# Kernel tuning notes

Measured on AMD Instinct MI355X. Metric: run time of the kernel, lower is better.

Reference implementation:

```python
import jax, jax.numpy as jnp
import numpy as np

B, TQ, TK = 2, 2048, 2048
D, H, G = 1024, 16, 4
HD = D // H  # 64
MAX_LEN = 4096


def _rope(x, max_len):
    # x: [B, H, S, hd]; interleaved even/odd RoPE, freqs use full head_dim in denom
    hd = x.shape[-1]
    seq = x.shape[2]
    pos = jnp.arange(max_len, dtype=jnp.float32)[:, None]           # [max_len, 1]
    div = jnp.exp(jnp.arange(0, hd, 2, dtype=jnp.float32) * (-np.log(10000.0) / hd))
    sin = jnp.sin(pos * div)[:seq]                                   # [S, hd/2]
    cos = jnp.cos(pos * div)[:seq]
    xe, xo = x[..., 0::2], x[..., 1::2]
    oe = xe * cos - xo * sin
    oo = xe * sin + xo * cos
    return jnp.stack([oe, oo], axis=-1).reshape(x.shape)


def setup_inputs() -> dict:
    key = jax.random.key(0)
    ks = jax.random.split(key, 10)
    s = 0.02
    return {
        "X": jax.random.normal(ks[0], (B, TQ, D), jnp.float32),
        "encoder_output": jax.random.normal(ks[1], (B, TK, D), jnp.float32),
        "Wq": jax.random.normal(ks[2], (D, D), jnp.float32) * s,
        "bq": jnp.zeros((D,), jnp.float32),
        "Wk": jax.random.normal(ks[3], (D, G * HD), jnp.float32) * s,
        "bk": jnp.zeros((G * HD,), jnp.float32),
        "Wv": jax.random.normal(ks[4], (D, G * HD), jnp.float32) * s,
        "bv": jnp.zeros((G * HD,), jnp.float32),
        "Wo": jax.random.normal(ks[5], (D, D), jnp.float32) * s,
        "bo": jnp.zeros((D,), jnp.float32),
        "max_len": MAX_LEN,
    }


def reference(X, encoder_output, Wq, bq, Wk, bk, Wv, bv, Wo, bo, max_len):
    bsz, tq, d = X.shape
    q = X @ Wq + bq                       # [B, TQ, D]
    k = encoder_output @ Wk + bk          # [B, TK, G*HD]
    v = encoder_output @ Wv + bv

    q = q.reshape(bsz, tq, H, HD).transpose(0, 2, 1, 3)          # [B, H, TQ, HD]
    k = k.reshape(bsz, -1, G, HD).transpose(0, 2, 1, 3)          # [B, G, TK, HD]
    v = v.reshape(bsz, -1, G, HD).transpose(0, 2, 1, 3)
    # expand each group to H//G consecutive heads (matches torch expand+reshape)
    k = jnp.repeat(k, H // G, axis=1)                            # [B, H, TK, HD]
    v = jnp.repeat(v, H // G, axis=1)

    q = _rope(q, max_len)
    k = _rope(k, max_len)

    scores = jnp.einsum("bhqd,bhkd->bhqk", q, k) / jnp.sqrt(jnp.float32(HD))
    w = jax.nn.softmax(scores, axis=-1)
    o = jnp.einsum("bhqk,bhkd->bhqd", w, v)                      # [B, H, TQ, HD]
    o = o.transpose(0, 2, 1, 3).reshape(bsz, tq, d)
    return o @ Wo + bo
```

## Files before the change

kernel.cpp:

```cpp
#include <hip/hip_runtime.h>
#include <cstdint>


typedef __bf16 bf16x8 __attribute__((ext_vector_type(8)));
typedef __bf16 bf16x4v __attribute__((ext_vector_type(4)));
typedef float f32x4 __attribute__((ext_vector_type(4)));

#define MFMA16(a, b, c) __builtin_amdgcn_mfma_f32_16x16x32_bf16((a), (b), (c), 0, 0, 0)

constexpr int Bc = 2, TQc = 2048, TKc = 2048, Dc = 1024, Hc = 16, Gc = 4, HDc = 64;
constexpr float QSCALE = 0.18033688011112042f;

__device__ __forceinline__ ushort bfbits(float x) {
  __bf16 h = (__bf16)x;
  return __builtin_bit_cast(ushort, h);
}

__device__ __forceinline__ float fexp2(float x) {
  float r;
  asm("v_exp_f32 %0, %1" : "=v"(r) : "v"(x));
  return r;
}

__device__ __forceinline__ float fmax3(float a, float b, float c) {
  return fmaxf(fmaxf(a, b), c);
}

__device__ __forceinline__ void async_lds16(void* lds, const void* g) {
  __builtin_amdgcn_global_load_lds((const __attribute__((address_space(1))) uint32_t*)g,
                                   (__attribute__((address_space(3))) uint32_t*)lds,
                                   16, 0, 0);
}

__global__ __launch_bounds__(256) void prep_k(const float* __restrict__ X,
                                              const float* __restrict__ E,
                                              const float* __restrict__ Wq,
                                              const float* __restrict__ Wo,
                                              const float* __restrict__ Wk,
                                              const float* __restrict__ Wv,
                                              ushort* __restrict__ Xb,
                                              ushort* __restrict__ Eb,
                                              ushort* __restrict__ Wqt,
                                              ushort* __restrict__ Wot,
                                              ushort* __restrict__ Wkvt) {
  __shared__ float t[64][65];
  const int bid = blockIdx.x;
  if (bid < 8192) {
    const float* s = (bid < 4096) ? X : E;
    ushort* d = (bid < 4096) ? Xb : Eb;
    int i = (bid & 4095) * 256 + threadIdx.x;
    float4 v = reinterpret_cast<const float4*>(s)[i];
    ushort4 o;
    o.x = bfbits(v.x); o.y = bfbits(v.y); o.z = bfbits(v.z); o.w = bfbits(v.w);
    reinterpret_cast<ushort4*>(d)[i] = o;
    return;
  }
  const int w = bid - 8192;
  const int z = w >> 8, rem = w & 255;
  const int bx = rem & 15, by = rem >> 4;
  const float* src;
  ushort* dst;
  int C, c0;
  if (z == 0)      { src = Wq; dst = Wqt; C = 1024; c0 = bx * 64; }
  else if (z == 1) { src = Wo; dst = Wot; C = 1024; c0 = bx * 64; }
  else {
    if (bx >= 8) return;
    if (bx < 4) { src = Wk; dst = Wkvt; }
    else        { src = Wv; dst = Wkvt + 256 * 1024; }
    C = 256; c0 = (bx & 3) * 64;
  }
  const int r0 = by * 64;
  const int tx = threadIdx.x & 63, ty = threadIdx.x >> 6;
#pragma unroll
  for (int i = 0; i < 16; ++i) {
    int r = i * 4 + ty;
    t[r][tx] = src[(size_t)(r0 + r) * C + c0 + tx];
  }
  __syncthreads();
#pragma unroll
  for (int i = 0; i < 16; ++i) {
    int c = i * 4 + ty;
    dst[(size_t)(c0 + c) * 1024 + r0 + tx] = bfbits(t[tx][c]);
  }
}

__device__ __forceinline__ void gemm_mainloop(const ushort* __restrict__ A,
                                              const ushort* __restrict__ Bt,
                                              int m0, int n0, int K,
                                              char* sA, char* sB,
                                              f32x4 acc[4][2]) {
  const int lane = threadIdx.x & 63, wid = threadIdx.x >> 6;
  const int l15 = lane & 15, l4 = lane >> 4;
  const int wr = (wid >> 1) * 64, wc = (wid & 1) * 32;
  const int srow = lane >> 3;
  const int scc = (lane & 7) ^ (srow & 7);
  const int rxr = l15 & 7;

  const int nsteps = K >> 6;
#pragma unroll
  for (int j = 0; j < 4; ++j) {
    int c = wid * 4 + j;
    async_lds16(sA + c * 1024, A + (size_t)(m0 + c * 8 + srow) * K + scc * 8);
  }
#pragma unroll
  for (int j = 0; j < 2; ++j) {
    int c = wid * 2 + j;
    async_lds16(sB + c * 1024, Bt + (size_t)(n0 + c * 8 + srow) * K + scc * 8);
  }
  __syncthreads();

  int buf = 0;
  for (int s2 = 0; s2 < nsteps; ++s2) {
    if (s2 + 1 < nsteps) {
      const int k0 = (s2 + 1) * 64;
      char* dA = sA + (buf ^ 1) * 16384;
      char* dB = sB + (buf ^ 1) * 8192;
#pragma unroll
      for (int j = 0; j < 4; ++j) {
        int c = wid * 4 + j;
        async_lds16(dA + c * 1024, A + (size_t)(m0 + c * 8 + srow) * K + k0 + scc * 8);
      }
#pragma unroll
      for (int j = 0; j < 2; ++j) {
        int c = wid * 2 + j;
        async_lds16(dB + c * 1024, Bt + (size_t)(n0 + c * 8 + srow) * K + k0 + scc * 8);
      }
    }
    const char* aB = sA + buf * 16384;
    const char* bB = sB + buf * 8192;
    bf16x8 af[2][4], bfr[2][2];
#pragma unroll
    for (int mi = 0; mi < 4; ++mi) {
      const int row = wr + mi * 16 + l15;
#pragma unroll
      for (int kk = 0; kk < 2; ++kk)
        af[kk][mi] = *reinterpret_cast<const bf16x8*>(
            aB + row * 128 + (((l4 + kk * 4) ^ rxr) << 4));
    }
#pragma unroll
    for (int ni = 0; ni < 2; ++ni) {
      const int row = wc + ni * 16 + l15;
#pragma unroll
      for (int kk = 0; kk < 2; ++kk)
        bfr[kk][ni] = *reinterpret_cast<const bf16x8*>(
            bB + row * 128 + (((l4 + kk * 4) ^ rxr) << 4));
    }
#pragma unroll
    for (int kk = 0; kk < 2; ++kk)
#pragma unroll
      for (int mi = 0; mi < 4; ++mi)
#pragma unroll
        for (int ni = 0; ni < 2; ++ni)
          acc[mi][ni] = MFMA16(af[kk][mi], bfr[kk][ni], acc[mi][ni]);
    __syncthreads();
    buf ^= 1;
  }
}

__device__ __forceinline__ void gemm_epilogue(f32x4 acc[4][2], int mode, int m0,
                                              int n0, const float* b0,
                                              const float* b1, float* Cf,
                                              ushort* U0, ushort* U1, int N) {
  const int lane = threadIdx.x & 63, wid = threadIdx.x >> 6;
  const int l15 = lane & 15, l4 = lane >> 4;
  const int wr = (wid >> 1) * 64, wc = (wid & 1) * 32;
#pragma unroll
  for (int ni = 0; ni < 2; ++ni) {
    const int col = n0 + wc + ni * 16 + l15;
    if (mode == 0) {
      const float bv = b0[col];
#pragma unroll
      for (int mi = 0; mi < 4; ++mi) {
        const int rowb = m0 + wr + mi * 16 + l4 * 4;
#pragma unroll
        for (int r = 0; r < 4; ++r)
          Cf[(size_t)(rowb + r) * N + col] = acc[mi][ni][r] + bv;
      }
    } else if (mode == 1) {
      const int h = col >> 6, d = col & 63, fi = d >> 1, odd = d & 1;
      const float div = __expf(-0.28782313662425572f * (float)fi);
      const float bv = b0[col];
#pragma unroll
      for (int mi = 0; mi < 4; ++mi) {
        const int rowb = m0 + wr + mi * 16 + l4 * 4;
#pragma unroll
        for (int r = 0; r < 4; ++r) {
          const int row = rowb + r, b = row >> 11, t = row & 2047;
          const float val = acc[mi][ni][r] + bv;
          const float prt = __shfl_xor(val, 1);
          float sn, cs;
          __sincosf((float)t * div, &sn, &cs);
          const float o = odd ? (prt * sn + val * cs) : (val * cs - prt * sn);
          U0[(((size_t)(b * Hc + h)) * TQc + t) * HDc + d] = bfbits(o * QSCALE);
        }
      }
    } else {
      if (col < 256) {
        const int g = col >> 6, d = col & 63, fi = d >> 1, odd = d & 1;
        const float div = __expf(-0.28782313662425572f * (float)fi);
        const float bv = b0[col];
#pragma unroll
        for (int mi = 0; mi < 4; ++mi) {
          const int rowb = m0 + wr + mi * 16 + l4 * 4;
#pragma unroll
          for (int r = 0; r < 4; ++r) {
            const int row = rowb + r, b = row >> 11, t = row & 2047;
            const float val = acc[mi][ni][r] + bv;
            const float prt = __shfl_xor(val, 1);
            float sn, cs;
            __sincosf((float)t * div, &sn, &cs);
            const float o = odd ? (prt * sn + val * cs) : (val * cs - prt * sn);
            U0[(((size_t)(b * Gc + g)) * TKc + t) * HDc + d] = bfbits(o);
          }
        }
      } else {
        const int c2 = col - 256;
        const int g = c2 >> 6, d = c2 & 63;
        const float bv = b1[c2];
#pragma unroll
        for (int mi = 0; mi < 4; ++mi) {
          const int rowb = m0 + wr + mi * 16 + l4 * 4;
          const int b = rowb >> 11, t0 = rowb & 2047;
          ushort4 w;
          w.x = bfbits(acc[mi][ni][0] + bv);
          w.y = bfbits(acc[mi][ni][1] + bv);
          w.z = bfbits(acc[mi][ni][2] + bv);
          w.w = bfbits(acc[mi][ni][3] + bv);
          *reinterpret_cast<ushort4*>(
              &U1[(((size_t)(b * Gc + g)) * HDc + d) * TKc + t0]) = w;
        }
      }
    }
  }
}

__global__ __launch_bounds__(256) void qkv_k(const ushort* __restrict__ Xb,
                                             const ushort* __restrict__ Eb,
                                             const ushort* __restrict__ Wqt,
                                             const ushort* __restrict__ Wkvt,
                                             const float* __restrict__ bq,
                                             const float* __restrict__ bk,
                                             const float* __restrict__ bv,
                                             ushort* __restrict__ Qb,
                                             ushort* __restrict__ Kb,
                                             ushort* __restrict__ Vt) {
  __shared__ __attribute__((aligned(16))) char smem[48 * 1024];
  const int bid = blockIdx.x;
  const ushort *A, *Bt;
  const float *b0, *b1 = nullptr;
  ushort *U0, *U1 = nullptr;
  int mode, tb, tn;
  if (bid < 512) { A = Xb; Bt = Wqt; b0 = bq; U0 = Qb; mode = 1; tb = bid; tn = 16; }
  else { A = Eb; Bt = Wkvt; b0 = bk; b1 = bv; U0 = Kb; U1 = Vt; mode = 2; tb = bid - 512; tn = 8; }
  const int m0 = (tb / tn) * 128, n0 = (tb % tn) * 64;
  const f32x4 z = {0.f, 0.f, 0.f, 0.f};
  f32x4 acc[4][2] = {{z, z}, {z, z}, {z, z}, {z, z}};
  gemm_mainloop(A, Bt, m0, n0, 1024, smem, smem + 32768, acc);
  gemm_epilogue(acc, mode, m0, n0, b0, b1, nullptr, U0, U1, 0);
}

__global__ __launch_bounds__(256) void oproj_k(const ushort* __restrict__ Ob,
                                               const ushort* __restrict__ Wot,
                                               const float* __restrict__ bo,
                                               float* __restrict__ out) {
  __shared__ __attribute__((aligned(16))) char smem[48 * 1024];
  const int bid = blockIdx.x;
  const int m0 = (bid >> 4) * 128, n0 = (bid & 15) * 64;
  const f32x4 z = {0.f, 0.f, 0.f, 0.f};
  f32x4 acc[4][2] = {{z, z}, {z, z}, {z, z}, {z, z}};
  gemm_mainloop(Ob, Wot, m0, n0, 1024, smem, smem + 32768, acc);
  gemm_epilogue(acc, 0, m0, n0, bo, nullptr, out, nullptr, nullptr, 1024);
}

__global__ __launch_bounds__(512, 4) void attn_k(const ushort* __restrict__ Qg,
                                                 const ushort* __restrict__ Kg,
                                                 const ushort* __restrict__ Vg,
                                                 ushort* __restrict__ Ob) {
  __shared__ __attribute__((aligned(16))) char smem[64 * 1024];
  const int lane = threadIdx.x & 63, wid = threadIdx.x >> 6;
  const int l15 = lane & 15, l4 = lane >> 4;
  const int bid = blockIdx.x;
  const int bg = bid & 7, pos = bid >> 3;
  const int b = bg >> 2, g = bg & 3;
  const int h = g * 4 + (pos >> 4);
  const int q0 = (pos & 15) * 128 + wid * 16;
  const ushort* Qp = Qg + ((size_t)(b * Hc + h)) * TQc * HDc;
  const ushort* Kp = Kg + ((size_t)(b * Gc + g)) * TKc * HDc;
  const ushort* Vp = Vg + ((size_t)(b * Gc + g)) * HDc * TKc;
  char* k0 = smem;
  char* k1 = smem + 8192;
  char* k2 = smem + 16384;
  char* v0 = smem + 24576;
  char* v1 = smem + 32768;
  char* v2 = smem + 40960;
  char* pb = smem + 49152 + wid * 2048;
  const int rx = (l15 & 7) << 4;
  const int swz = l15 & 7;

  const int sr = wid * 8 + (lane >> 3);
  const int sc = (lane & 7) ^ ((lane >> 3) & 7);
  const char* KstN = (const char*)Kp + (size_t)sr * 128 + sc * 16;
  const char* VstN = (const char*)Vp + (size_t)sr * (TKc * 2) + sc * 16;

  bf16x8 bq0 = *reinterpret_cast<const bf16x8*>(Qp + (size_t)(q0 + l15) * HDc + l4 * 8);
  bf16x8 bq1 = *reinterpret_cast<const bf16x8*>(Qp + (size_t)(q0 + l15) * HDc + 32 + l4 * 8);

  float m = -INFINITY, l = 0.f;
  const f32x4 z = {0.f, 0.f, 0.f, 0.f};
  f32x4 accO[4] = {z, z, z, z};

  constexpr int NT = TKc / 64;
  async_lds16(k0 + wid * 1024, KstN);
  async_lds16(v0 + wid * 1024, VstN);
  KstN += 8192; VstN += 128;
  async_lds16(k1 + wid * 1024, KstN);
  async_lds16(v1 + wid * 1024, VstN);
  KstN += 8192; VstN += 128;

  for (int kt = 0; kt < NT; ++kt) {
    if (kt < NT - 1) asm volatile("s_waitcnt vmcnt(2)" ::: "memory");
    else             asm volatile("s_waitcnt vmcnt(0)" ::: "memory");
    __builtin_amdgcn_s_barrier();
    __builtin_amdgcn_sched_barrier(0);
    if (kt + 2 < NT) {
      async_lds16(k2 + wid * 1024, KstN);
      async_lds16(v2 + wid * 1024, VstN);
      KstN += 8192; VstN += 128;
    }

    f32x4 s[4] = {z, z, z, z};
#pragma unroll
    for (int nf = 0; nf < 4; ++nf) {
      const char* krow = k0 + (nf * 16 + l15) * 128;
      bf16x8 kf0 = *reinterpret_cast<const bf16x8*>(krow + ((l4 ^ swz) << 4));
      bf16x8 kf1 = *reinterpret_cast<const bf16x8*>(krow + (((4 + l4) ^ swz) << 4));
      s[nf] = MFMA16(kf0, bq0, s[nf]);
      s[nf] = MFMA16(kf1, bq1, s[nf]);
    }
    bf16x8 va[4][2];
#pragma unroll
    for (int df = 0; df < 4; ++df) {
      const char* vrow = v0 + (df * 16 + l15) * 128;
      va[df][0] = *reinterpret_cast<const bf16x8*>(vrow + ((l4 ^ swz) << 4));
      va[df][1] = *reinterpret_cast<const bf16x8*>(vrow + (((4 + l4) ^ swz) << 4));
    }

    float pm = fmax3(fmax3(s[0][0], s[0][1], s[0][2]),
                     fmax3(s[0][3], s[1][0], s[1][1]),
                     fmax3(s[1][2], s[1][3], s[2][0]));
    pm = fmax3(pm,
               fmax3(s[2][1], s[2][2], s[2][3]),
               fmax3(s[3][0], s[3][1], fmaxf(s[3][2], s[3][3])));
    pm = fmaxf(pm, __shfl_xor(pm, 16));
    pm = fmaxf(pm, __shfl_xor(pm, 32));
    if (!__all(pm - m <= 11.5f)) {
      float mn = fmaxf(m, pm);
      float sc2 = fexp2(m - mn);
      m = mn;
      l *= sc2;
#pragma unroll
      for (int df = 0; df < 4; ++df) accO[df] *= sc2;
    }
    float ps = 0.f;
#pragma unroll
    for (int nf = 0; nf < 4; ++nf)
#pragma unroll
      for (int r = 0; r < 4; ++r) {
        float p = fexp2(s[nf][r] - m);
        s[nf][r] = p;
        ps += p;
      }
    ps += __shfl_xor(ps, 16);
    ps += __shfl_xor(ps, 32);
    l += ps;

#pragma unroll
    for (int nf = 0; nf < 4; ++nf) {
      bf16x4v pv;
      pv[0] = (__bf16)s[nf][0];
      pv[1] = (__bf16)s[nf][1];
      pv[2] = (__bf16)s[nf][2];
      pv[3] = (__bf16)s[nf][3];
      *reinterpret_cast<uint2*>(pb + l15 * 128 + ((nf * 32 + l4 * 8) ^ rx)) =
          __builtin_bit_cast(uint2, pv);
    }
    asm volatile("" ::: "memory");
    bf16x8 ap0 = *reinterpret_cast<const bf16x8*>(pb + l15 * 128 + ((l4 * 16) ^ rx));
    bf16x8 ap1 = *reinterpret_cast<const bf16x8*>(pb + l15 * 128 + ((64 + l4 * 16) ^ rx));
#pragma unroll
    for (int df = 0; df < 4; ++df)
      accO[df] = MFMA16(ap1, va[df][1], MFMA16(ap0, va[df][0], accO[df]));

    char* tk = k0; k0 = k1; k1 = k2; k2 = tk;
    char* tv = v0; v0 = v1; v1 = v2; v2 = tv;
  }

  float inv[4];
#pragma unroll
  for (int r = 0; r < 4; ++r) inv[r] = 1.f / __shfl(l, l4 * 4 + r);
#pragma unroll
  for (int df = 0; df < 4; ++df)
#pragma unroll
    for (int r = 0; r < 4; ++r) {
      int row = q0 + l4 * 4 + r;
      int col = h * HDc + df * 16 + l15;
      Ob[((size_t)b * TQc + row) * Dc + col] = bfbits(accO[df][r] * inv[r]);
    }
}

extern "C" void kernel_launch(void* const* d_in, const int* in_sizes, int n_in,
                              void* d_out, int out_size, void* d_ws, size_t ws_size,
                              hipStream_t stream) {
  const float* X  = (const float*)d_in[0];
  const float* E  = (const float*)d_in[1];
  const float* Wq = (const float*)d_in[2];
  const float* bq = (const float*)d_in[3];
  const float* Wk = (const float*)d_in[4];
  const float* bk = (const float*)d_in[5];
  const float* Wv = (const float*)d_in[6];
  const float* bv = (const float*)d_in[7];
  const float* Wo = (const float*)d_in[8];
  const float* bo = (const float*)d_in[9];
  float* out = (float*)d_out;
  char* ws = (char*)d_ws;

  const size_t MB = 1ull << 20;
  if (ws_size < 42 * MB) return;

  ushort* Xb   = (ushort*)(ws + 0 * MB);
  ushort* Eb   = (ushort*)(ws + 8 * MB);
  ushort* Wqt  = (ushort*)(ws + 16 * MB);
  ushort* Wkvt = (ushort*)(ws + 18 * MB);
  ushort* Wot  = (ushort*)(ws + 19 * MB);
  ushort* Qb   = (ushort*)(ws + 21 * MB);
  ushort* Kb   = (ushort*)(ws + 29 * MB);
  ushort* Vt   = (ushort*)(ws + 31 * MB);
  ushort* Ob   = (ushort*)(ws + 33 * MB);

  prep_k<<<dim3(8960), 256, 0, stream>>>(X, E, Wq, Wo, Wk, Wv, Xb, Eb, Wqt, Wot, Wkvt);
  qkv_k<<<dim3(768), 256, 0, stream>>>(Xb, Eb, Wqt, Wkvt, bq, bk, bv, Qb, Kb, Vt);
  attn_k<<<dim3(512), dim3(512), 0, stream>>>(Qb, Kb, Vt, Ob);
  oproj_k<<<dim3(512), 256, 0, stream>>>(Ob, Wot, bo, out);
}
```

Before: 105.5 us.

## Triple-buffer GEMM mainloop and compute softmax row sums via MFMA

The GEMM mainloop moves from a double-buffered LDS scheme with two __syncthreads per step to a three-stage ring. It issues loads two steps ahead and uses a vmcnt wait plus a single barrier per step, which raises LDS per block to 72KB. Separately, the attention kernel drops the scalar exp-sum and its cross-lane shuffles, and computes the row sums with an extra MFMA of P against a ones vector. The sums are then taken from bf16-rounded P values, and the larger LDS footprint may lower GEMM occupancy.

```diff
diff --git a/kernel.cpp b/kernel.cpp
--- a/kernel.cpp
+++ b/kernel.cpp
@@ -87,8 +87,7 @@
 __device__ __forceinline__ void gemm_mainloop(const ushort* __restrict__ A,
                                               const ushort* __restrict__ Bt,
                                               int m0, int n0, int K,
-                                              char* sA, char* sB,
-                                              f32x4 acc[4][2]) {
+                                              char* smem, f32x4 acc[4][2]) {
   const int lane = threadIdx.x & 63, wid = threadIdx.x >> 6;
   const int l15 = lane & 15, l4 = lane >> 4;
   const int wr = (wid >> 1) * 64, wc = (wid & 1) * 32;
@@ -96,38 +95,38 @@
   const int scc = (lane & 7) ^ (srow & 7);
   const int rxr = l15 & 7;
 
+  char* bufA[3] = {smem, smem + 24576, smem + 49152};
+  char* bufB[3] = {smem + 16384, smem + 40960, smem + 65536};
+
+  auto stage = [&](int step, int bi) {
+    const int k0 = step * 64;
+    char* dA = bufA[bi];
+    char* dB = bufB[bi];
+#pragma unroll
+    for (int j = 0; j < 4; ++j) {
+      int c = wid * 4 + j;
+      async_lds16(dA + c * 1024, A + (size_t)(m0 + c * 8 + srow) * K + k0 + scc * 8);
+    }
+#pragma unroll
+    for (int j = 0; j < 2; ++j) {
+      int c = wid * 2 + j;
+      async_lds16(dB + c * 1024, Bt + (size_t)(n0 + c * 8 + srow) * K + k0 + scc * 8);
+    }
+  };
+
   const int nsteps = K >> 6;
-#pragma unroll
-  for (int j = 0; j < 4; ++j) {
-    int c = wid * 4 + j;
-    async_lds16(sA + c * 1024, A + (size_t)(m0 + c * 8 + srow) * K + scc * 8);
-  }
-#pragma unroll
-  for (int j = 0; j < 2; ++j) {
-    int c = wid * 2 + j;
-    async_lds16(sB + c * 1024, Bt + (size_t)(n0 + c * 8 + srow) * K + scc * 8);
-  }
-  __syncthreads();
-
-  int buf = 0;
+  stage(0, 0);
+  stage(1, 1);
+  int cur = 0, nxt = 2;
   for (int s2 = 0; s2 < nsteps; ++s2) {
-    if (s2 + 1 < nsteps) {
-      const int k0 = (s2 + 1) * 64;
-      char* dA = sA + (buf ^ 1) * 16384;
-      char* dB = sB + (buf ^ 1) * 8192;
-#pragma unroll
-      for (int j = 0; j < 4; ++j) {
-        int c = wid * 4 + j;
-        async_lds16(dA + c * 1024, A + (size_t)(m0 + c * 8 + srow) * K + k0 + scc * 8);
-      }
-#pragma unroll
-      for (int j = 0; j < 2; ++j) {
-        int c = wid * 2 + j;
-        async_lds16(dB + c * 1024, Bt + (size_t)(n0 + c * 8 + srow) * K + k0 + scc * 8);
-      }
-    }
-    const char* aB = sA + buf * 16384;
-    const char* bB = sB + buf * 8192;
+    if (s2 + 1 < nsteps) asm volatile("s_waitcnt vmcnt(6)" ::: "memory");
+    else                 asm volatile("s_waitcnt vmcnt(0)" ::: "memory");
+    __builtin_amdgcn_s_barrier();
+    __builtin_amdgcn_sched_barrier(0);
+    if (s2 + 2 < nsteps) stage(s2 + 2, nxt);
+
+    const char* aB = bufA[cur];
+    const char* bB = bufB[cur];
     bf16x8 af[2][4], bfr[2][2];
 #pragma unroll
     for (int mi = 0; mi < 4; ++mi) {
@@ -152,8 +151,9 @@
 #pragma unroll
         for (int ni = 0; ni < 2; ++ni)
           acc[mi][ni] = MFMA16(af[kk][mi], bfr[kk][ni], acc[mi][ni]);
-    __syncthreads();
-    buf ^= 1;
+
+    cur = (cur == 2) ? 0 : cur + 1;
+    nxt = (nxt == 2) ? 0 : nxt + 1;
   }
 }
 
@@ -244,7 +244,7 @@
                                              ushort* __restrict__ Qb,
                                              ushort* __restrict__ Kb,
                                              ushort* __restrict__ Vt) {
-  __shared__ __attribute__((aligned(16))) char smem[48 * 1024];
+  __shared__ __attribute__((aligned(16))) char smem[72 * 1024];
   const int bid = blockIdx.x;
   const ushort *A, *Bt;
   const float *b0, *b1 = nullptr;
@@ -255,7 +255,7 @@
   const int m0 = (tb / tn) * 128, n0 = (tb % tn) * 64;
   const f32x4 z = {0.f, 0.f, 0.f, 0.f};
   f32x4 acc[4][2] = {{z, z}, {z, z}, {z, z}, {z, z}};
-  gemm_mainloop(A, Bt, m0, n0, 1024, smem, smem + 32768, acc);
+  gemm_mainloop(A, Bt, m0, n0, 1024, smem, acc);
   gemm_epilogue(acc, mode, m0, n0, b0, b1, nullptr, U0, U1, 0);
 }
 
@@ -263,12 +263,12 @@
                                                const ushort* __restrict__ Wot,
                                                const float* __restrict__ bo,
                                                float* __restrict__ out) {
-  __shared__ __attribute__((aligned(16))) char smem[48 * 1024];
+  __shared__ __attribute__((aligned(16))) char smem[72 * 1024];
   const int bid = blockIdx.x;
   const int m0 = (bid >> 4) * 128, n0 = (bid & 15) * 64;
   const f32x4 z = {0.f, 0.f, 0.f, 0.f};
   f32x4 acc[4][2] = {{z, z}, {z, z}, {z, z}, {z, z}};
-  gemm_mainloop(Ob, Wot, m0, n0, 1024, smem, smem + 32768, acc);
+  gemm_mainloop(Ob, Wot, m0, n0, 1024, smem, acc);
   gemm_epilogue(acc, 0, m0, n0, bo, nullptr, out, nullptr, nullptr, 1024);
 }
 
@@ -305,9 +305,14 @@
   bf16x8 bq0 = *reinterpret_cast<const bf16x8*>(Qp + (size_t)(q0 + l15) * HDc + l4 * 8);
   bf16x8 bq1 = *reinterpret_cast<const bf16x8*>(Qp + (size_t)(q0 + l15) * HDc + 32 + l4 * 8);
 
-  float m = -INFINITY, l = 0.f;
+  bf16x8 vones;
+#pragma unroll
+  for (int i = 0; i < 8; ++i) vones[i] = (__bf16)1.0f;
+
+  float m = -INFINITY;
   const f32x4 z = {0.f, 0.f, 0.f, 0.f};
   f32x4 accO[4] = {z, z, z, z};
+  f32x4 acc1 = z;
 
   constexpr int NT = TKc / 64;
   async_lds16(k0 + wid * 1024, KstN);
@@ -357,22 +362,15 @@
       float mn = fmaxf(m, pm);
       float sc2 = fexp2(m - mn);
       m = mn;
-      l *= sc2;
+      acc1 *= sc2;
 #pragma unroll
       for (int df = 0; df < 4; ++df) accO[df] *= sc2;
     }
-    float ps = 0.f;
 #pragma unroll
     for (int nf = 0; nf < 4; ++nf)
 #pragma unroll
-      for (int r = 0; r < 4; ++r) {
-        float p = fexp2(s[nf][r] - m);
-        s[nf][r] = p;
-        ps += p;
-      }
-    ps += __shfl_xor(ps, 16);
-    ps += __shfl_xor(ps, 32);
-    l += ps;
+      for (int r = 0; r < 4; ++r)
+        s[nf][r] = fexp2(s[nf][r] - m);
 
 #pragma unroll
     for (int nf = 0; nf < 4; ++nf) {
@@ -390,6 +388,7 @@
 #pragma unroll
     for (int df = 0; df < 4; ++df)
       accO[df] = MFMA16(ap1, va[df][1], MFMA16(ap0, va[df][0], accO[df]));
+    acc1 = MFMA16(ap1, vones, MFMA16(ap0, vones, acc1));
 
     char* tk = k0; k0 = k1; k1 = k2; k2 = tk;
     char* tv = v0; v0 = v1; v1 = v2; v2 = tv;
@@ -397,7 +396,7 @@
 
   float inv[4];
 #pragma unroll
-  for (int r = 0; r < 4; ++r) inv[r] = 1.f / __shfl(l, l4 * 4 + r);
+  for (int r = 0; r < 4; ++r) inv[r] = 1.f / acc1[r];
 #pragma unroll
   for (int df = 0; df < 4; ++df)
 #pragma unroll
```

Result: slower. 123.7 us (+17.3%).
